# Kernel tuning notes

Hardware: AMD Instinct MI355X
Metric: run time of the kernel (lower is better)

Reference implementation:

```python
import jax, jax.numpy as jnp
import numpy as np

EMBED_DIM = 1024
NUM_HEADS = 16
HEAD_DIM = EMBED_DIM // NUM_HEADS
D_FF = 4096
N, T, S = 4, 2048, 2048


def _linear_params(key, d_in, d_out):
    k1, k2 = jax.random.split(key)
    bound = 1.0 / np.sqrt(d_in)
    W = jax.random.uniform(k1, (d_in, d_out), minval=-bound, maxval=bound, dtype=jnp.float32)
    b = jax.random.uniform(k2, (d_out,), minval=-bound, maxval=bound, dtype=jnp.float32)
    return W, b


def setup_inputs() -> dict:
    key = jax.random.key(0)
    ks = jax.random.split(key, 20)
    inp = {
        'tgt': jax.random.normal(ks[0], (N, T, EMBED_DIM), dtype=jnp.float32),
        'memory': jax.random.normal(ks[1], (N, S, EMBED_DIM), dtype=jnp.float32),
        'tgt_mask': jnp.tril(jnp.ones((T, T), dtype=jnp.float32)),
    }
    # self-attn params
    for i, nm in enumerate(['sa_Wq', 'sa_Wk', 'sa_Wv', 'sa_A', 'ca_Wq', 'ca_Wk', 'ca_Wv', 'ca_A']):
        W, b = _linear_params(ks[2 + i], EMBED_DIM, EMBED_DIM)
        inp[nm] = W
        inp[nm + '_b'] = b
    W1, b1 = _linear_params(ks[10], EMBED_DIM, D_FF)
    W2, b2 = _linear_params(ks[11], D_FF, EMBED_DIM)
    inp.update(lin1_W=W1, lin1_b=b1, lin2_W=W2, lin2_b=b2)
    for i in (1, 2, 3):
        inp[f'ln{i}_g'] = jnp.ones((EMBED_DIM,), dtype=jnp.float32)
        inp[f'ln{i}_b'] = jnp.zeros((EMBED_DIM,), dtype=jnp.float32)
    return inp


def _layer_norm(x, g, b, eps=1e-5):
    mu = jnp.mean(x, axis=-1, keepdims=True)
    var = jnp.var(x, axis=-1, keepdims=True)
    return (x - mu) * jax.lax.rsqrt(var + eps) * g + b


def _mha(query, key, value, Wq, bq, Wk, bk, Wv, bv, Wa, ba, mask=None):
    Nq, Tq, D = query.shape
    Tk = key.shape[1]
    q = (query @ Wq + bq).reshape(Nq, Tq, NUM_HEADS, HEAD_DIM)
    k = (key @ Wk + bk).reshape(Nq, Tk, NUM_HEADS, HEAD_DIM)
    v = (value @ Wv + bv).reshape(Nq, Tk, NUM_HEADS, HEAD_DIM)
    attn = jnp.einsum('bthd,bshd->bhts', q, k) / np.sqrt(HEAD_DIM)
    if mask is not None:
        attn = jnp.where(mask == 0, -jnp.inf, attn)
    score = jax.nn.softmax(attn, axis=-1)
    y = jnp.einsum('bhts,bshd->bthd', score, v).reshape(Nq, Tq, D)
    return y @ Wa + ba


def reference(tgt, memory, tgt_mask,
              sa_Wq, sa_Wq_b, sa_Wk, sa_Wk_b, sa_Wv, sa_Wv_b, sa_A, sa_A_b,
              ca_Wq, ca_Wq_b, ca_Wk, ca_Wk_b, ca_Wv, ca_Wv_b, ca_A, ca_A_b,
              lin1_W, lin1_b, lin2_W, lin2_b,
              ln1_g, ln1_b, ln2_g, ln2_b, ln3_g, ln3_b):
    t2 = _mha(tgt, tgt, tgt, sa_Wq, sa_Wq_b, sa_Wk, sa_Wk_b, sa_Wv, sa_Wv_b, sa_A, sa_A_b, tgt_mask)
    x = _layer_norm(tgt + t2, ln1_g, ln1_b)
    t2 = _mha(x, memory, memory, ca_Wq, ca_Wq_b, ca_Wk, ca_Wk_b, ca_Wv, ca_Wv_b, ca_A, ca_A_b)
    x = _layer_norm(x + t2, ln2_g, ln2_b)
    t2 = jax.nn.relu(x @ lin1_W + lin1_b) @ lin2_W + lin2_b
    return _layer_norm(x + t2, ln3_g, ln3_b)
```

## Files before the change

kernel.cpp:

```cpp
#include <hip/hip_runtime.h>

typedef __bf16 bf16;
typedef __bf16 bf16x4 __attribute__((ext_vector_type(4)));
typedef __bf16 bf16x8 __attribute__((ext_vector_type(8)));
typedef float  f32x4  __attribute__((ext_vector_type(4)));

#define EMBED 1024
#define HEADS 16
#define HDIM  64
#define DFF   4096
#define BATCH 4
#define SEQ   2048
#define MROWS 8192

__global__ __launch_bounds__(256) void cvt_kernel(
    const float* __restrict__ x, bf16* __restrict__ y, int n)
{
  int i = (blockIdx.x * 256 + threadIdx.x) * 8;
  if (i >= n) return;
  float4 a = *(const float4*)(x + i);
  float4 b = *(const float4*)(x + i + 4);
  bf16x8 v;
  v[0] = (bf16)a.x; v[1] = (bf16)a.y; v[2] = (bf16)a.z; v[3] = (bf16)a.w;
  v[4] = (bf16)b.x; v[5] = (bf16)b.y; v[6] = (bf16)b.z; v[7] = (bf16)b.w;
  *(bf16x8*)(y + i) = v;
}

__global__ __launch_bounds__(256) void wt_kernel(
    const float* __restrict__ W, bf16* __restrict__ Wt, int K, int N)
{
  __shared__ __align__(16) float Ls[64 * 68];
  const int k0 = blockIdx.x * 64, n0 = blockIdx.y * 64;
  const int ty = threadIdx.x >> 4, tx = threadIdx.x & 15;
  #pragma unroll
  for (int r = 0; r < 4; ++r) {
    const int k = ty + r * 16;
    float4 v = *(const float4*)(W + (size_t)(k0 + k) * N + n0 + tx * 4);
    *(float4*)(Ls + k * 68 + tx * 4) = v;
  }
  __syncthreads();
  #pragma unroll
  for (int it = 0; it < 2; ++it) {
    const int c = it * 256 + threadIdx.x;
    const int n = c >> 3, kc = (c & 7) * 8;
    bf16x8 v;
    #pragma unroll
    for (int j = 0; j < 8; ++j) v[j] = (bf16)Ls[(kc + j) * 68 + n];
    *(bf16x8*)(Wt + (size_t)(n0 + n) * K + k0 + kc) = v;
  }
}

__global__ void cat3_kernel(float* __restrict__ dst, const float* __restrict__ a,
                            const float* __restrict__ b, const float* __restrict__ c, int n)
{
  int i = blockIdx.x * 256 + threadIdx.x;
  if (i < n) dst[i] = a[i];
  else if (i < 2 * n) dst[i] = b[i - n];
  else if (c && i < 3 * n) dst[i] = c[i - 2 * n];
}

__global__ __launch_bounds__(256) void vtr_kernel(
    const bf16* __restrict__ V, int ldv, bf16* __restrict__ Vt, int Skv)
{
  __shared__ __align__(16) bf16 Ls[64 * 72];
  const int k0 = blockIdx.x * 64;
  const int bh = blockIdx.y, b = bh >> 4, h = bh & 15;
  const int t = threadIdx.x;
  {
    const int key = t >> 2, dc = (t & 3) * 16;
    const bf16* src = V + (size_t)(b * Skv + k0 + key) * ldv + h * HDIM + dc;
    bf16x8 a0 = *(const bf16x8*)src;
    bf16x8 a1 = *(const bf16x8*)(src + 8);
    *(bf16x8*)(Ls + key * 72 + dc) = a0;
    *(bf16x8*)(Ls + key * 72 + dc + 8) = a1;
  }
  __syncthreads();
  {
    const int d = t >> 2, kc = (t & 3) * 16;
    bf16x8 v0, v1;
    #pragma unroll
    for (int j = 0; j < 8; ++j) v0[j] = Ls[(kc + j) * 72 + d];
    #pragma unroll
    for (int j = 0; j < 8; ++j) v1[j] = Ls[(kc + 8 + j) * 72 + d];
    bf16* dst = Vt + ((size_t)(bh * HDIM + d)) * Skv + k0 + kc;
    *(bf16x8*)dst = v0;
    *(bf16x8*)(dst + 8) = v1;
  }
}

__device__ __forceinline__ void gll16(const bf16* g, bf16* l) {
  __builtin_amdgcn_global_load_lds(
      (const __attribute__((address_space(1))) unsigned*)g,
      (__attribute__((address_space(3))) unsigned*)l, 16, 0, 0);
}

__global__ __launch_bounds__(256) void gemm128(
    const bf16* __restrict__ A, int lda, const bf16* __restrict__ Bt, int ldb,
    const float* __restrict__ bias, const bf16* __restrict__ res_b,
    const float* __restrict__ res_f, bf16* __restrict__ out_b,
    float* __restrict__ out_f, int N, int K, int relu)
{
  __shared__ __align__(16) bf16 As[3][128 * 32];
  __shared__ __align__(16) bf16 Bs[3][128 * 32];
  const int tid  = threadIdx.x;
  const int lane = tid & 63, wave = tid >> 6;
  const int quad = lane >> 4, l16 = lane & 15;
  const int wm = wave & 1, wn = wave >> 1;

  const int gx   = gridDim.x;
  const int nwg  = gx * gridDim.y;
  const int flat = blockIdx.y * gx + blockIdx.x;
  const int wg   = (flat & 7) * (nwg >> 3) + (flat >> 3);
  const int m0 = (wg / gx) * 128, n0 = (wg % gx) * 128;

  const int c0row = tid >> 2, c0kc = (tid & 3) * 8;
  const int c1row = 64 + c0row;

  const bf16* a0 = A  + (size_t)(m0 + c0row) * lda + c0kc;
  const bf16* b0 = Bt + (size_t)(n0 + c0row) * ldb + c0kc;
  const bf16* a1 = A  + (size_t)(m0 + c1row) * lda + c0kc;
  const bf16* b1 = Bt + (size_t)(n0 + c1row) * ldb + c0kc;

  f32x4 acc[4][4];
  #pragma unroll
  for (int i = 0; i < 4; ++i)
    #pragma unroll
    for (int j = 0; j < 4; ++j) acc[i][j] = f32x4{0, 0, 0, 0};

  auto stage = [&](int k0, int buf) {
    gll16(a0 + k0, As[buf] + wave * 512);
    gll16(b0 + k0, Bs[buf] + wave * 512);
    gll16(a1 + k0, As[buf] + 2048 + wave * 512);
    gll16(b1 + k0, Bs[buf] + 2048 + wave * 512);
  };

  const int nk = K >> 5;
  stage(0, 0);
  if (nk > 1) stage(32, 1);

  int cur = 0;
  for (int t = 0; t < nk; ++t) {
    if (t + 1 < nk) asm volatile("s_waitcnt vmcnt(4)" ::: "memory");
    else            asm volatile("s_waitcnt vmcnt(0)" ::: "memory");
    __builtin_amdgcn_s_barrier();
    __builtin_amdgcn_sched_barrier(0);

    bf16x8 af[4], bfr[4];
    #pragma unroll
    for (int i = 0; i < 4; ++i)
      af[i] = *(const bf16x8*)(As[cur] + (wm * 64 + i * 16 + l16) * 32 + quad * 8);
    #pragma unroll
    for (int j = 0; j < 4; ++j)
      bfr[j] = *(const bf16x8*)(Bs[cur] + (wn * 64 + j * 16 + l16) * 32 + quad * 8);
    #pragma unroll
    for (int i = 0; i < 4; ++i)
      #pragma unroll
      for (int j = 0; j < 4; ++j)
        acc[i][j] = __builtin_amdgcn_mfma_f32_16x16x32_bf16(af[i], bfr[j], acc[i][j], 0, 0, 0);

    if (t + 2 < nk) {
      int nb = cur + 2; if (nb >= 3) nb -= 3;
      stage((t + 2) << 5, nb);
    }
    cur = (cur + 1 == 3) ? 0 : cur + 1;
  }

  #pragma unroll
  for (int j = 0; j < 4; ++j) {
    const int col = n0 + wn * 64 + j * 16 + l16;
    const float bv = bias ? bias[col] : 0.f;
    #pragma unroll
    for (int i = 0; i < 4; ++i) {
      #pragma unroll
      for (int r = 0; r < 4; ++r) {
        const int row = m0 + wm * 64 + i * 16 + quad * 4 + r;
        const size_t idx = (size_t)row * N + col;
        float v = acc[i][j][r] + bv;
        if (res_b) v += (float)res_b[idx];
        if (res_f) v += res_f[idx];
        if (relu)  v = fmaxf(v, 0.f);
        if (out_b) out_b[idx] = (bf16)v;
        if (out_f) out_f[idx] = v;
      }
    }
  }
}

__global__ __launch_bounds__(256) void ln_kernel(
    const float* __restrict__ x, const float* __restrict__ g, const float* __restrict__ b,
    bf16* __restrict__ out_b, float* __restrict__ out_f)
{
  __shared__ float red[8];
  const int tid = threadIdx.x, lane = tid & 63, wave = tid >> 6;
  const float* xr = x + (size_t)blockIdx.x * EMBED;
  float4 v = *(const float4*)(xr + tid * 4);
  float vv[4] = {v.x, v.y, v.z, v.w};
  float s  = vv[0] + vv[1] + vv[2] + vv[3];
  float s2 = vv[0]*vv[0] + vv[1]*vv[1] + vv[2]*vv[2] + vv[3]*vv[3];
  #pragma unroll
  for (int off = 32; off >= 1; off >>= 1) {
    s  += __shfl_xor(s, off);
    s2 += __shfl_xor(s2, off);
  }
  if (lane == 0) { red[wave] = s; red[4 + wave] = s2; }
  __syncthreads();
  s  = red[0] + red[1] + red[2] + red[3];
  s2 = red[4] + red[5] + red[6] + red[7];
  const float mu  = s * (1.f / EMBED);
  const float var = s2 * (1.f / EMBED) - mu * mu;
  const float rs  = rsqrtf(fmaxf(var, 0.f) + 1e-5f);
  #pragma unroll
  for (int i = 0; i < 4; ++i) {
    const int col = tid * 4 + i;
    const float o = (vv[i] - mu) * rs * g[col] + b[col];
    const size_t idx = (size_t)blockIdx.x * EMBED + col;
    if (out_b) out_b[idx] = (bf16)o;
    if (out_f) out_f[idx] = o;
  }
}

__global__ __launch_bounds__(256) void fattn_kernel(
    const bf16* __restrict__ Q, int ldq, const bf16* __restrict__ K, int ldk,
    const bf16* __restrict__ Vt, bf16* __restrict__ Y, int Skv, int causal)
{
  constexpr int PLD = 72;
  __shared__ __align__(16) bf16 Ks[2][64 * 64];
  __shared__ __align__(16) bf16 Vs[2][64 * 64];
  __shared__ __align__(16) bf16 Ps[4 * 32 * PLD];

  const int tid  = threadIdx.x;
  const int lane = tid & 63, wave = tid >> 6;
  const int quad = lane >> 4, l16 = lane & 15;
  const int bh = blockIdx.y, b = bh >> 4, h = bh & 15;

  const bf16* Kb = K + (size_t)b * Skv * ldk + h * HDIM;
  const bf16* Vb = Vt + (size_t)(bh * HDIM) * Skv;

  const int sr = lane >> 3;
  const int se = ((lane & 7) ^ sr) << 3;

  const int sw  = l16 & 7;
  const int co0 = (quad ^ sw) << 3;
  const int co1 = ((4 + quad) ^ sw) << 3;

  auto stage = [&](int kt, int buf) {
    const int k0 = kt * 64;
    const int r0 = wave * 16;
    gll16(Kb + (size_t)(k0 + r0 + sr) * ldk + se,     &Ks[buf][(r0)     * 64]);
    gll16(Kb + (size_t)(k0 + r0 + 8 + sr) * ldk + se, &Ks[buf][(r0 + 8) * 64]);
    gll16(Vb + (size_t)(r0 + sr) * Skv + k0 + se,     &Vs[buf][(r0)     * 64]);
    gll16(Vb + (size_t)(r0 + 8 + sr) * Skv + k0 + se, &Vs[buf][(r0 + 8) * 64]);
  };

  bf16* Pw = Ps + wave * 32 * PLD;
  const int npass = causal ? 2 : 1;

  for (int pass = 0; pass < npass; ++pass) {
    const int qt = causal ? (pass == 0 ? (int)blockIdx.x
                                       : (SEQ / 128 - 1 - (int)blockIdx.x))
                          : (int)blockIdx.x;
    const int q0  = qt * 128;
    const int wq0 = q0 + wave * 32;

    bf16x8 qf[2][2];
    #pragma unroll
    for (int i = 0; i < 2; ++i) {
      const bf16* qp = Q + (size_t)(b * SEQ + wq0 + i * 16 + l16) * ldq + h * HDIM;
      qf[i][0] = *(const bf16x8*)(qp + quad * 8);
      qf[i][1] = *(const bf16x8*)(qp + 32 + quad * 8);
    }

    f32x4 O[2][4];
    float m_run[2], l_run[2];
    #pragma unroll
    for (int i = 0; i < 2; ++i)
      #pragma unroll
      for (int nt = 0; nt < 4; ++nt) O[i][nt] = f32x4{0, 0, 0, 0};
    #pragma unroll
    for (int i = 0; i < 2; ++i) { m_run[i] = -1e30f; l_run[i] = 0.f; }

    const int nkt = causal ? (q0 / 64 + 2) : (Skv / 64);

    stage(0, 0);
    __syncthreads();

    for (int kt = 0; kt < nkt; ++kt) {
      const int cur = kt & 1;
      const int k0 = kt * 64;
      if (kt + 1 < nkt) stage(kt + 1, cur ^ 1);

      const bf16* Kc = Ks[cur];
      const bf16* Vc = Vs[cur];

      f32x4 s[2][4];
      __builtin_amdgcn_s_setprio(1);
      #pragma unroll
      for (int nt = 0; nt < 4; ++nt) {
        const int row = nt * 16 + l16;
        bf16x8 kf0 = *(const bf16x8*)(Kc + row * 64 + co0);
        bf16x8 kf1 = *(const bf16x8*)(Kc + row * 64 + co1);
        #pragma unroll
        for (int i = 0; i < 2; ++i) {
          f32x4 t = f32x4{0, 0, 0, 0};
          t = __builtin_amdgcn_mfma_f32_16x16x32_bf16(kf0, qf[i][0], t, 0, 0, 0);
          t = __builtin_amdgcn_mfma_f32_16x16x32_bf16(kf1, qf[i][1], t, 0, 0, 0);
          s[i][nt] = t;
        }
      }
      __builtin_amdgcn_s_setprio(0);

      if (causal && (k0 + 63 > wq0)) {
        #pragma unroll
        for (int i = 0; i < 2; ++i) {
          const int q = wq0 + i * 16 + l16;
          #pragma unroll
          for (int nt = 0; nt < 4; ++nt) {
            #pragma unroll
            for (int r = 0; r < 4; ++r) {
              const int key = k0 + nt * 16 + quad * 4 + r;
              if (key > q) s[i][nt][r] = -1e30f;
            }
          }
        }
      }

      #pragma unroll
      for (int i = 0; i < 2; ++i) {
        float pm = s[i][0][0];
        #pragma unroll
        for (int nt = 0; nt < 4; ++nt)
          #pragma unroll
          for (int r = 0; r < 4; ++r) pm = fmaxf(pm, s[i][nt][r]);
        pm = fmaxf(pm, __shfl_xor(pm, 16));
        pm = fmaxf(pm, __shfl_xor(pm, 32));
        const float m_new = fmaxf(m_run[i], pm);
        const float al = __expf((m_run[i] - m_new) * 0.125f);
        m_run[i] = m_new;
        const float mc = m_new * 0.125f;
        float ls = 0.f;
        #pragma unroll
        for (int nt = 0; nt < 4; ++nt) {
          #pragma unroll
          for (int r = 0; r < 4; ++r) {
            const float e = __expf(fmaf(s[i][nt][r], 0.125f, -mc));
            s[i][nt][r] = e;
            ls += e;
          }
        }
        ls += __shfl_xor(ls, 16);
        ls += __shfl_xor(ls, 32);
        l_run[i] = l_run[i] * al + ls;
        #pragma unroll
        for (int nt = 0; nt < 4; ++nt) {
          bf16x4 pk;
          pk[0] = (bf16)s[i][nt][0]; pk[1] = (bf16)s[i][nt][1];
          pk[2] = (bf16)s[i][nt][2]; pk[3] = (bf16)s[i][nt][3];
          *(bf16x4*)(Pw + (i * 16 + l16) * PLD + nt * 16 + quad * 4) = pk;
        }
        float alo[4];
        #pragma unroll
        for (int r = 0; r < 4; ++r) alo[r] = __shfl(al, quad * 4 + r);
        #pragma unroll
        for (int nt = 0; nt < 4; ++nt)
          #pragma unroll
          for (int r = 0; r < 4; ++r) O[i][nt][r] *= alo[r];
      }

      bf16x8 pf[2][2];
      #pragma unroll
      for (int i = 0; i < 2; ++i) {
        pf[i][0] = *(const bf16x8*)(Pw + (i * 16 + l16) * PLD + quad * 8);
        pf[i][1] = *(const bf16x8*)(Pw + (i * 16 + l16) * PLD + 32 + quad * 8);
      }
      __builtin_amdgcn_s_setprio(1);
      #pragma unroll
      for (int nt = 0; nt < 4; ++nt) {
        const int row = nt * 16 + l16;
        bf16x8 vf0 = *(const bf16x8*)(Vc + row * 64 + co0);
        bf16x8 vf1 = *(const bf16x8*)(Vc + row * 64 + co1);
        #pragma unroll
        for (int i = 0; i < 2; ++i) {
          O[i][nt] = __builtin_amdgcn_mfma_f32_16x16x32_bf16(pf[i][0], vf0, O[i][nt], 0, 0, 0);
          O[i][nt] = __builtin_amdgcn_mfma_f32_16x16x32_bf16(pf[i][1], vf1, O[i][nt], 0, 0, 0);
        }
      }
      __builtin_amdgcn_s_setprio(0);
      __syncthreads();
    }

    #pragma unroll
    for (int i = 0; i < 2; ++i) {
      float inv[4];
      #pragma unroll
      for (int r = 0; r < 4; ++r) {
        const float lv = __shfl(l_run[i], quad * 4 + r);
        inv[r] = 1.f / lv;
      }
      #pragma unroll
      for (int nt = 0; nt < 4; ++nt) {
        #pragma unroll
        for (int r = 0; r < 4; ++r) {
          const int q = wq0 + i * 16 + quad * 4 + r;
          Y[((size_t)(b * SEQ + q)) * EMBED + h * HDIM + nt * 16 + l16] = (bf16)(O[i][nt][r] * inv[r]);
        }
      }
    }
  }
}

__global__ void fill_kernel(float* out, float v, int n) {
  int i = blockIdx.x * 256 + threadIdx.x;
  if (i < n) out[i] = v;
}

extern "C" void kernel_launch(void* const* d_in, const int* in_sizes, int n_in,
                              void* d_out, int out_size, void* d_ws, size_t ws_size,
                              hipStream_t stream)
{
  const float* tgt    = (const float*)d_in[0];
  const float* mem    = (const float*)d_in[1];
  const float* sa_Wq  = (const float*)d_in[3];
  const float* sa_Wqb = (const float*)d_in[4];
  const float* sa_Wk  = (const float*)d_in[5];
  const float* sa_Wkb = (const float*)d_in[6];
  const float* sa_Wv  = (const float*)d_in[7];
  const float* sa_Wvb = (const float*)d_in[8];
  const float* sa_A   = (const float*)d_in[9];
  const float* sa_Ab  = (const float*)d_in[10];
  const float* ca_Wq  = (const float*)d_in[11];
  const float* ca_Wqb = (const float*)d_in[12];
  const float* ca_Wk  = (const float*)d_in[13];
  const float* ca_Wkb = (const float*)d_in[14];
  const float* ca_Wv  = (const float*)d_in[15];
  const float* ca_Wvb = (const float*)d_in[16];
  const float* ca_A   = (const float*)d_in[17];
  const float* ca_Ab  = (const float*)d_in[18];
  const float* l1W    = (const float*)d_in[19];
  const float* l1b    = (const float*)d_in[20];
  const float* l2W    = (const float*)d_in[21];
  const float* l2b    = (const float*)d_in[22];
  const float* g1     = (const float*)d_in[23];
  const float* b1     = (const float*)d_in[24];
  const float* g2     = (const float*)d_in[25];
  const float* b2     = (const float*)d_in[26];
  const float* g3     = (const float*)d_in[27];
  const float* b3     = (const float*)d_in[28];

  const size_t MB = 1024 * 1024;
  const size_t NEED = 80 * MB + 4096;
  if (ws_size < NEED) {
    fill_kernel<<<(out_size + 255) / 256, 256, 0, stream>>>((float*)d_out, 3.0f, out_size);
    return;
  }

  char* ws = (char*)d_ws;
  const size_t MD = (size_t)MROWS * EMBED;
  bf16*  qkv   = (bf16*)ws;
  bf16*  yb    = (bf16*)(ws + 48 * MB);
  bf16*  wqkvt = (bf16*)(ws + 48 * MB);
  float* qkvbias = (float*)(ws + 54 * MB + 512 * 1024);
  bf16*  kvb   = (bf16*)ws;
  bf16*  qB    = (bf16*)(ws + 32 * MB);
  bf16*  wkvt  = (bf16*)(ws + 48 * MB);
  bf16*  wqt   = (bf16*)(ws + 52 * MB);
  float* kvbias = (float*)(ws + 54 * MB + 512 * 1024);
  bf16*  awt   = (bf16*)ws;
  bf16*  xb    = (bf16*)(ws + 64 * MB);
  bf16*  hb    = (bf16*)ws;
  bf16*  l1t   = (bf16*)(ws + 32 * MB);
  bf16*  l2t   = (bf16*)(ws + 40 * MB);
  float* P   = (float*)d_out;
  bf16*  inb = (bf16*)d_out;
  bf16*  vtg = (bf16*)((char*)d_out + 16 * MB);

  dim3 blk(256);
  dim3 gQKV(3072 / 128, MROWS / 128);
  dim3 gKV(2048 / 128, MROWS / 128);
  dim3 gEE(EMBED / 128, MROWS / 128);
  dim3 gF1(2048 / 128, MROWS / 128);
  dim3 gATC(SEQ / 256, BATCH * HEADS);
  dim3 gAT(SEQ / 128, BATCH * HEADS);
  dim3 gVT(SEQ / 64, BATCH * HEADS);
  dim3 gWee(16, 16);
  const int ncv = (int)(MD / 8 / 256);

  cvt_kernel<<<ncv, blk, 0, stream>>>(tgt, inb, (int)MD);
  wt_kernel<<<gWee, blk, 0, stream>>>(sa_Wq, wqkvt, EMBED, EMBED);
  wt_kernel<<<gWee, blk, 0, stream>>>(sa_Wk, wqkvt + 1024 * 1024, EMBED, EMBED);
  wt_kernel<<<gWee, blk, 0, stream>>>(sa_Wv, wqkvt + 2 * 1024 * 1024, EMBED, EMBED);
  cat3_kernel<<<12, blk, 0, stream>>>(qkvbias, sa_Wqb, sa_Wkb, sa_Wvb, EMBED);
  gemm128<<<gQKV, blk, 0, stream>>>(inb, EMBED, wqkvt, EMBED, qkvbias, nullptr, nullptr, qkv, nullptr, 3072, EMBED, 0);
  vtr_kernel<<<gVT, blk, 0, stream>>>(qkv + 2048, 3072, vtg, SEQ);
  fattn_kernel<<<gATC, blk, 0, stream>>>(qkv, 3072, qkv + 1024, 3072, vtg, yb, SEQ, 1);
  wt_kernel<<<gWee, blk, 0, stream>>>(sa_A, awt, EMBED, EMBED);
  gemm128<<<gEE, blk, 0, stream>>>(yb, EMBED, awt, EMBED, sa_Ab, nullptr, tgt, nullptr, P, EMBED, EMBED, 0);
  ln_kernel<<<MROWS, blk, 0, stream>>>(P, g1, b1, xb, nullptr);

  cvt_kernel<<<ncv, blk, 0, stream>>>(mem, inb, (int)MD);
  wt_kernel<<<gWee, blk, 0, stream>>>(ca_Wk, wkvt, EMBED, EMBED);
  wt_kernel<<<gWee, blk, 0, stream>>>(ca_Wv, wkvt + 1024 * 1024, EMBED, EMBED);
  wt_kernel<<<gWee, blk, 0, stream>>>(ca_Wq, wqt, EMBED, EMBED);
  cat3_kernel<<<8, blk, 0, stream>>>(kvbias, ca_Wkb, ca_Wvb, nullptr, EMBED);
  gemm128<<<gKV, blk, 0, stream>>>(inb, EMBED, wkvt, EMBED, kvbias, nullptr, nullptr, kvb, nullptr, 2048, EMBED, 0);
  gemm128<<<gEE, blk, 0, stream>>>(xb, EMBED, wqt, EMBED, ca_Wqb, nullptr, nullptr, qB, nullptr, EMBED, EMBED, 0);
  vtr_kernel<<<gVT, blk, 0, stream>>>(kvb + 1024, 2048, vtg, SEQ);
  fattn_kernel<<<gAT, blk, 0, stream>>>(qB, 1024, kvb, 2048, vtg, yb, SEQ, 0);
  wt_kernel<<<gWee, blk, 0, stream>>>(ca_A, awt, EMBED, EMBED);
  gemm128<<<gEE, blk, 0, stream>>>(yb, EMBED, awt, EMBED, ca_Ab, xb, nullptr, nullptr, P, EMBED, EMBED, 0);
  ln_kernel<<<MROWS, blk, 0, stream>>>(P, g2, b2, xb, nullptr);

  wt_kernel<<<dim3(16, 64), blk, 0, stream>>>(l1W, l1t, EMBED, DFF);
  wt_kernel<<<dim3(64, 16), blk, 0, stream>>>(l2W, l2t, DFF, EMBED);
  gemm128<<<gF1, blk, 0, stream>>>(xb, EMBED, l1t, EMBED, l1b, nullptr, nullptr, hb, nullptr, 2048, EMBED, 1);
  gemm128<<<gEE, blk, 0, stream>>>(hb, 2048, l2t, DFF, l2b, xb, nullptr, nullptr, P, EMBED, 2048, 0);
  gemm128<<<gF1, blk, 0, stream>>>(xb, EMBED, l1t + (size_t)2048 * 1024, EMBED, l1b + 2048, nullptr, nullptr, hb, nullptr, 2048, EMBED, 1);
  gemm128<<<gEE, blk, 0, stream>>>(hb, 2048, l2t + 2048, DFF, nullptr, nullptr, P, nullptr, P, EMBED, 2048, 0);
  ln_kernel<<<MROWS, blk, 0, stream>>>(P, g3, b3, nullptr, (float*)d_out);
}
```

Baseline: 1.019 ms.

## Load K/V fragments directly from global memory in flash attention, dropping LDS staging

The attention kernel no longer double-buffers K and V tiles through shared memory with async global-to-LDS loads and barriers. Each wave now reads its K and V MFMA fragments straight from global memory into registers every iteration, and the per-iteration __syncthreads goes away. This removes LDS traffic and synchronisation but makes the four waves each fetch the same K/V data, relying on L2/L1 for reuse. Load latency is no longer hidden by prefetching and register pressure goes up.

```diff
diff --git a/kernel.cpp b/kernel.cpp
--- a/kernel.cpp
+++ b/kernel.cpp
@@ -224,8 +224,6 @@
     const bf16* __restrict__ Vt, bf16* __restrict__ Y, int Skv, int causal)
 {
   constexpr int PLD = 72;
-  __shared__ __align__(16) bf16 Ks[2][64 * 64];
-  __shared__ __align__(16) bf16 Vs[2][64 * 64];
   __shared__ __align__(16) bf16 Ps[4 * 32 * PLD];
 
   const int tid  = threadIdx.x;
@@ -235,22 +233,6 @@
 
   const bf16* Kb = K + (size_t)b * Skv * ldk + h * HDIM;
   const bf16* Vb = Vt + (size_t)(bh * HDIM) * Skv;
-
-  const int sr = lane >> 3;
-  const int se = ((lane & 7) ^ sr) << 3;
-
-  const int sw  = l16 & 7;
-  const int co0 = (quad ^ sw) << 3;
-  const int co1 = ((4 + quad) ^ sw) << 3;
-
-  auto stage = [&](int kt, int buf) {
-    const int k0 = kt * 64;
-    const int r0 = wave * 16;
-    gll16(Kb + (size_t)(k0 + r0 + sr) * ldk + se,     &Ks[buf][(r0)     * 64]);
-    gll16(Kb + (size_t)(k0 + r0 + 8 + sr) * ldk + se, &Ks[buf][(r0 + 8) * 64]);
-    gll16(Vb + (size_t)(r0 + sr) * Skv + k0 + se,     &Vs[buf][(r0)     * 64]);
-    gll16(Vb + (size_t)(r0 + 8 + sr) * Skv + k0 + se, &Vs[buf][(r0 + 8) * 64]);
-  };
 
   bf16* Pw = Ps + wave * 32 * PLD;
   const int npass = causal ? 2 : 1;
@@ -281,33 +263,38 @@
 
     const int nkt = causal ? (q0 / 64 + 2) : (Skv / 64);
 
-    stage(0, 0);
-    __syncthreads();
-
     for (int kt = 0; kt < nkt; ++kt) {
-      const int cur = kt & 1;
       const int k0 = kt * 64;
-      if (kt + 1 < nkt) stage(kt + 1, cur ^ 1);
-
-      const bf16* Kc = Ks[cur];
-      const bf16* Vc = Vs[cur];
+
+      bf16x8 kf[4][2];
+      #pragma unroll
+      for (int nt = 0; nt < 4; ++nt) {
+        const bf16* kp = Kb + (size_t)(k0 + nt * 16 + l16) * ldk + quad * 8;
+        kf[nt][0] = *(const bf16x8*)kp;
+        kf[nt][1] = *(const bf16x8*)(kp + 32);
+      }
 
       f32x4 s[2][4];
       __builtin_amdgcn_s_setprio(1);
       #pragma unroll
       for (int nt = 0; nt < 4; ++nt) {
-        const int row = nt * 16 + l16;
-        bf16x8 kf0 = *(const bf16x8*)(Kc + row * 64 + co0);
-        bf16x8 kf1 = *(const bf16x8*)(Kc + row * 64 + co1);
         #pragma unroll
         for (int i = 0; i < 2; ++i) {
           f32x4 t = f32x4{0, 0, 0, 0};
-          t = __builtin_amdgcn_mfma_f32_16x16x32_bf16(kf0, qf[i][0], t, 0, 0, 0);
-          t = __builtin_amdgcn_mfma_f32_16x16x32_bf16(kf1, qf[i][1], t, 0, 0, 0);
+          t = __builtin_amdgcn_mfma_f32_16x16x32_bf16(kf[nt][0], qf[i][0], t, 0, 0, 0);
+          t = __builtin_amdgcn_mfma_f32_16x16x32_bf16(kf[nt][1], qf[i][1], t, 0, 0, 0);
           s[i][nt] = t;
         }
       }
       __builtin_amdgcn_s_setprio(0);
+
+      bf16x8 vf[4][2];
+      #pragma unroll
+      for (int nt = 0; nt < 4; ++nt) {
+        const bf16* vp = Vb + (size_t)(nt * 16 + l16) * Skv + k0 + quad * 8;
+        vf[nt][0] = *(const bf16x8*)vp;
+        vf[nt][1] = *(const bf16x8*)(vp + 32);
+      }
 
       if (causal && (k0 + 63 > wq0)) {
         #pragma unroll
@@ -375,17 +362,13 @@
       __builtin_amdgcn_s_setprio(1);
       #pragma unroll
       for (int nt = 0; nt < 4; ++nt) {
-        const int row = nt * 16 + l16;
-        bf16x8 vf0 = *(const bf16x8*)(Vc + row * 64 + co0);
-        bf16x8 vf1 = *(const bf16x8*)(Vc + row * 64 + co1);
         #pragma unroll
         for (int i = 0; i < 2; ++i) {
-          O[i][nt] = __builtin_amdgcn_mfma_f32_16x16x32_bf16(pf[i][0], vf0, O[i][nt], 0, 0, 0);
-          O[i][nt] = __builtin_amdgcn_mfma_f32_16x16x32_bf16(pf[i][1], vf1, O[i][nt], 0, 0, 0);
+          O[i][nt] = __builtin_amdgcn_mfma_f32_16x16x32_bf16(pf[i][0], vf[nt][0], O[i][nt], 0, 0, 0);
+          O[i][nt] = __builtin_amdgcn_mfma_f32_16x16x32_bf16(pf[i][1], vf[nt][1], O[i][nt], 0, 0, 0);
         }
       }
       __builtin_amdgcn_s_setprio(0);
-      __syncthreads();
     }
 
     #pragma unroll
```

After: 1.139 ms. +11.7%, slower.
